# Performance work log

Measured on AMD Instinct MI355X. Metric: run time of the kernel, lower is better.

The kernel has to match this reference:

```python
import jax, jax.numpy as jnp
import numpy as np

B, T, HU, C = 256, 128, 512, 64

def setup_inputs() -> dict:
    key = jax.random.key(0)
    k = jax.random.split(key, 8)
    H = jax.random.normal(k[0], (B, T, HU), dtype=jnp.float32)
    y = jax.random.randint(k[1], (B, T), 0, C)
    y_len = jax.random.randint(k[2], (B,), 1, T + 1).astype(jnp.int32)
    y_mask = (jnp.arange(T)[None, :] < y_len[:, None]).astype(jnp.float32)
    xav = float(np.sqrt(6.0 / (3 * HU + C)))
    W = jax.random.uniform(k[3], (C, 3 * HU), minval=-xav, maxval=xav, dtype=jnp.float32)
    b = jnp.zeros((C,), dtype=jnp.float32)
    start_transitions = jax.random.uniform(k[4], (C,), minval=-1.0, maxval=1.0, dtype=jnp.float32)
    end_transitions = jax.random.uniform(k[5], (C,), minval=-1.0, maxval=1.0, dtype=jnp.float32)
    transitions = jax.random.uniform(k[6], (C, C), minval=-1.0, maxval=1.0, dtype=jnp.float32)
    return {"H": H, "W": W, "b": b, "start_transitions": start_transitions,
            "end_transitions": end_transitions, "transitions": transitions,
            "y": y, "y_mask": y_mask, "y_len": y_len}

def _crf_ll(H, W, b, start_transitions, end_transitions, transitions, y, y_mask, y_len):
    Bn, Tn, hu = H.shape
    zeros = jnp.zeros((Bn, 1, hu), H.dtype)
    prev = jnp.concatenate([zeros, H[:, :-1, :]], axis=1)
    nxt = jnp.concatenate([H[:, 1:, :], zeros], axis=1)
    context = jnp.concatenate([prev, H, nxt], axis=-1)            # [B,T,3h]
    scores = jnp.einsum('bth,ch->btc', context, W) + b            # [B,T,C]

    # numerator (gold path score)
    em_sel = jnp.take_along_axis(scores, y[..., None], axis=2)[..., 0]  # [B,T]
    num = start_transitions[y[:, 0]]
    num = num + jnp.sum(em_sel[:, :-1] * y_mask[:, :-1], axis=1)
    num = num + jnp.sum(transitions[y[:, :-1], y[:, 1:]] * y_mask[:, 1:], axis=1)
    last_tags = jnp.take_along_axis(y, (y_len - 1)[:, None].astype(y.dtype), axis=1)[:, 0]
    num = num + end_transitions[last_tags]
    num = num + jnp.take_along_axis(scores[:, -1, :], last_tags[:, None], axis=1)[:, 0] * y_mask[:, -1]

    # partition (log Z) via masked logsumexp scan
    em_t = jnp.transpose(scores, (1, 0, 2))   # [T,B,C]
    m_t = y_mask.T                            # [T,B]
    lp0 = start_transitions[None, :] + em_t[0]
    def step(lp, inp):
        em, m = inp
        new = jax.nn.logsumexp(lp[:, :, None] + transitions[None, :, :] + em[:, None, :], axis=1)
        lp = new * m[:, None] + lp * (1.0 - m[:, None])
        return lp, None
    lp, _ = jax.lax.scan(step, lp0, (em_t[1:], m_t[1:]))
    logZ = jax.nn.logsumexp(lp + end_transitions[None, :], axis=1)
    return num - logZ                          # [B]

def reference(H, W, b, start_transitions, end_transitions, transitions, y, y_mask, y_len):
    return _crf_ll(H, W, b, start_transitions, end_transitions, transitions, y, y_mask, y_len)
```

## Files before the change

kernel.cpp:

```cpp
#include <hip/hip_runtime.h>

typedef __attribute__((ext_vector_type(8))) short short8;
typedef __attribute__((ext_vector_type(4))) float f32x4;
typedef __fp16 h2_t __attribute__((ext_vector_type(2)));

__device__ __forceinline__ unsigned pk_rtz(float a, float b) {
  h2_t h = __builtin_amdgcn_cvt_pkrtz(a, b);
  return __builtin_bit_cast(unsigned, h);
}
__device__ __forceinline__ unsigned pk_rne(float a, float b) {
  unsigned short ha = __builtin_bit_cast(unsigned short, (_Float16)a);
  unsigned short hb = __builtin_bit_cast(unsigned short, (_Float16)b);
  return (unsigned)ha | ((unsigned)hb << 16);
}
__device__ __forceinline__ unsigned short f2bf(float x) {
  unsigned int u = __float_as_uint(x);
  u += 0x7FFFu + ((u >> 16) & 1u);
  return (unsigned short)(u >> 16);
}
__device__ __forceinline__ unsigned scale_bf_pair(unsigned w, float s) {
  float f0 = __uint_as_float(w << 16) * s;
  float f1 = __uint_as_float(w & 0xFFFF0000u) * s;
  unsigned r;
  asm("v_cvt_pk_bf16_f32 %0, %1, %2" : "=v"(r) : "v"(f0), "v"(f1));
  return r;
}

__global__ __launch_bounds__(512) void crf_fused_kernel(
    const float* __restrict__ H, const float* __restrict__ W,
    const float* __restrict__ bias,
    const float* __restrict__ startT, const float* __restrict__ endT,
    const float* __restrict__ trans,
    const int* __restrict__ y, const int* __restrict__ y_len,
    float* __restrict__ out)
{
  __shared__ __align__(16) float smem[25088];
  __shared__ __align__(16) unsigned char EAbuf[8192];
  __shared__ __align__(16) float sc[128][68];
  __shared__ float scm[128];
  __shared__ float emy[128];
  __shared__ __align__(16) float ubuf[64];
  unsigned char* aTh = (unsigned char*)smem;
  unsigned char* aTl = aTh + 16384;
  unsigned char* bTh = aTh + 32768;
  float* P = smem;
  unsigned char* Mbase = (unsigned char*)smem;

  const int b    = blockIdx.x;
  const int tid  = threadIdx.x;
  const int lane = tid & 63;
  const int wid  = tid >> 6;
  const int wm   = wid >> 2;
  const int wn   = wid & 3;

  f32x4 acc[4][3] = {};
  const float* Hb = H + (size_t)b * (128 * 512);
  const int len = y_len[b];
  const int* yb = y + b * 128;

  float4 areg[4], breg[6];
  int aRow[4], aK4[4], bN[6], bK4[6];
  #pragma unroll
  for (int it = 0; it < 4; ++it) { int i = it * 512 + tid; aRow[it] = i >> 4; aK4[it] = i & 15; }
  #pragma unroll
  for (int it = 0; it < 6; ++it) { int i = it * 512 + tid; bN[it] = i >> 4; bK4[it] = i & 15; }
  #pragma unroll
  for (int it = 0; it < 4; ++it)
    areg[it] = ((const float4*)(Hb + aRow[it] * 512))[aK4[it]];
  #pragma unroll
  for (int it = 0; it < 6; ++it)
    breg[it] = ((const float4*)(W + (bN[it] & 63) * 1536 + (bN[it] >> 6) * 512))[bK4[it]];

  #pragma unroll
  for (int it = 0; it < 2; ++it) {
    int idx = it * 512 + tid;
    int c = idx >> 4, c4 = idx & 15;
    float4 v = ((const float4*)trans)[idx];
    #pragma unroll
    for (int e = 0; e < 4; ++e) {
      int cp = c4 * 4 + e;
      float val = __expf(((const float*)&v)[e] - 1.0f);
      *(unsigned short*)(EAbuf + cp * 128 + ((2 * c) ^ ((cp & 7) << 4))) = f2bf(val);
    }
  }

  for (int kk = 0; kk < 512; kk += 64) {
    if (kk) __syncthreads();
    #pragma unroll
    for (int it = 0; it < 4; ++it) {
      float4 v = areg[it];
      h2_t h01 = __builtin_amdgcn_cvt_pkrtz(v.x, v.y);
      h2_t h23 = __builtin_amdgcn_cvt_pkrtz(v.z, v.w);
      float r0 = v.x - (float)h01[0];
      float r1 = v.y - (float)h01[1];
      float r2 = v.z - (float)h23[0];
      float r3 = v.w - (float)h23[1];
      uint2 hi; hi.x = __builtin_bit_cast(unsigned, h01); hi.y = __builtin_bit_cast(unsigned, h23);
      uint2 lo; lo.x = pk_rtz(r0, r1); lo.y = pk_rtz(r2, r3);
      int off = aRow[it] * 128 + ((aK4[it] * 8) ^ ((aRow[it] & 7) << 4));
      *(uint2*)(aTh + off) = hi; *(uint2*)(aTl + off) = lo;
    }
    #pragma unroll
    for (int it = 0; it < 6; ++it) {
      float4 v = breg[it];
      uint2 bh; bh.x = pk_rne(v.x, v.y); bh.y = pk_rne(v.z, v.w);
      int off = bN[it] * 128 + ((bK4[it] * 8) ^ ((bN[it] & 7) << 4));
      *(uint2*)(bTh + off) = bh;
    }
    __syncthreads();
    if (kk < 448) {
      #pragma unroll
      for (int it = 0; it < 4; ++it)
        areg[it] = ((const float4*)(Hb + aRow[it] * 512 + kk + 64))[aK4[it]];
      #pragma unroll
      for (int it = 0; it < 6; ++it)
        breg[it] = ((const float4*)(W + (bN[it] & 63) * 1536 + (bN[it] >> 6) * 512 + kk + 64))[bK4[it]];
    }
    #pragma unroll
    for (int ks = 0; ks < 2; ++ks) {
      const int kbyte = ks * 64 + ((lane >> 4) << 4);
      short8 ah[4], al[4], bh[3];
      #pragma unroll
      for (int m = 0; m < 4; ++m) {
        int row = wm * 64 + m * 16 + (lane & 15);
        int off = row * 128 + (kbyte ^ ((row & 7) << 4));
        ah[m] = *(const short8*)(aTh + off);
        al[m] = *(const short8*)(aTl + off);
      }
      #pragma unroll
      for (int n = 0; n < 3; ++n) {
        int col = wn * 48 + n * 16 + (lane & 15);
        int off = col * 128 + (kbyte ^ ((col & 7) << 4));
        bh[n] = *(const short8*)(bTh + off);
      }
      #pragma unroll
      for (int m = 0; m < 4; ++m)
        #pragma unroll
        for (int n = 0; n < 3; ++n) {
          asm("v_mfma_f32_16x16x32_f16 %0, %1, %2, %0"
              : "+v"(acc[m][n]) : "v"(ah[m]), "v"(bh[n]));
          asm("v_mfma_f32_16x16x32_f16 %0, %1, %2, %0"
              : "+v"(acc[m][n]) : "v"(al[m]), "v"(bh[n]));
        }
    }
  }
  __syncthreads();

  #pragma unroll
  for (int m = 0; m < 4; ++m)
    #pragma unroll
    for (int n = 0; n < 3; ++n) {
      int row0 = wm * 64 + m * 16 + ((lane >> 4) << 2);
      int col  = wn * 48 + n * 16 + (lane & 15);
      #pragma unroll
      for (int j = 0; j < 4; ++j)
        P[(row0 + j) * 196 + col] = acc[m][n][j];
    }
  __syncthreads();

  #pragma unroll
  for (int it = 0; it < 4; ++it) {
    int i4 = it * 512 + tid;
    int t = i4 >> 4, c4 = i4 & 15;
    float4 s = *(const float4*)(P + t * 196 + 64 + c4 * 4);
    float4 bb = ((const float4*)bias)[c4];
    s.x += bb.x; s.y += bb.y; s.z += bb.z; s.w += bb.w;
    if (t > 0) {
      float4 g = *(const float4*)(P + (t - 1) * 196 + c4 * 4);
      s.x += g.x; s.y += g.y; s.z += g.z; s.w += g.w;
    }
    if (t < 127) {
      float4 g = *(const float4*)(P + (t + 1) * 196 + 128 + c4 * 4);
      s.x += g.x; s.y += g.y; s.z += g.z; s.w += g.w;
    }
    *(float4*)(&sc[t][c4 * 4]) = s;
    float m4 = fmaxf(fmaxf(s.x, s.y), fmaxf(s.z, s.w));
    #pragma unroll
    for (int o = 1; o < 16; o <<= 1) m4 = fmaxf(m4, __shfl_xor(m4, o, 64));
    if ((lane & 15) == 0) scm[t] = m4;
    int yt = yb[t];
    if ((yt >> 2) == c4) {
      int r = yt & 3;
      emy[t] = (r == 0) ? s.x : (r == 1) ? s.y : (r == 2) ? s.z : s.w;
    }
  }
  __syncthreads();

  {
    int row = tid >> 2, c0 = (tid & 3) << 4;
    float mt = scm[row];
    float4* p4 = (float4*)&sc[row][c0];
    #pragma unroll
    for (int j = 0; j < 4; ++j) {
      float4 x = p4[j];
      x.x = __expf(x.x - mt); x.y = __expf(x.y - mt);
      x.z = __expf(x.z - mt); x.w = __expf(x.w - mt);
      p4[j] = x;
    }
  }
  float num = 0.f;
  if (wid == 0) {
    float p = 0.f;
    #pragma unroll
    for (int rep = 0; rep < 2; ++rep) {
      int t = lane + rep * 64;
      if (t < 127) {
        int yt = yb[t], yt1 = yb[t + 1];
        if (t < len)     p += emy[t];
        if (t + 1 < len) p += trans[yt * 64 + yt1];
      }
    }
    #pragma unroll
    for (int s = 32; s > 0; s >>= 1) p += __shfl_xor(p, s, 64);
    num = p + startT[yb[0]] + endT[yb[len - 1]];
    if (len == 128) num += emy[127];
  }
  __syncthreads();

  {
    unsigned char* Mb = Mbase + wid * 8192;
    int t0 = (wid == 0) ? 1 : 16 * wid;
    int t1 = 16 * wid + 15; if (t1 > len - 1) t1 = len - 1;
    if (t0 <= t1) {
      const int sw = (lane & 7) << 4;
      float s0 = sc[t0][lane];
      #pragma unroll
      for (int j = 0; j < 8; ++j) {
        uint4 w = *(const uint4*)(EAbuf + lane * 128 + ((j * 16) ^ sw));
        uint4 o;
        o.x = scale_bf_pair(w.x, s0); o.y = scale_bf_pair(w.y, s0);
        o.z = scale_bf_pair(w.z, s0); o.w = scale_bf_pair(w.w, s0);
        *(uint4*)(Mb + lane * 128 + ((j * 16) ^ sw)) = o;
      }
      short8 ea[4][2];
      #pragma unroll
      for (int rt = 0; rt < 4; ++rt)
        #pragma unroll
        for (int kh = 0; kh < 2; ++kh) {
          int row = rt * 16 + (lane & 15);
          int kb = kh * 64 + ((lane >> 4) << 4);
          ea[rt][kh] = *(const short8*)(EAbuf + row * 128 + (kb ^ ((row & 7) << 4)));
        }
      f32x4 z4 = {0.f, 0.f, 0.f, 0.f};
      for (int t = t0 + 1; t <= t1; ++t) {
        short8 mf[4][2];
        #pragma unroll
        for (int ct = 0; ct < 4; ++ct)
          #pragma unroll
          for (int kh = 0; kh < 2; ++kh) {
            int row = ct * 16 + (lane & 15);
            int kb = kh * 64 + ((lane >> 4) << 4);
            mf[ct][kh] = *(const short8*)(Mb + row * 128 + (kb ^ ((row & 7) << 4)));
          }
        f32x4 sv[4];
        #pragma unroll
        for (int rt = 0; rt < 4; ++rt)
          sv[rt] = *(const f32x4*)(&sc[t][rt * 16 + ((lane >> 4) << 2)]);
        f32x4 c[4][4];
        #pragma unroll
        for (int rt = 0; rt < 4; ++rt)
          #pragma unroll
          for (int ct = 0; ct < 4; ++ct) {
            asm("v_mfma_f32_16x16x32_bf16 %0, %1, %2, %3"
                : "=&v"(c[rt][ct]) : "v"(ea[rt][0]), "v"(mf[ct][0]), "v"(z4));
            asm("v_mfma_f32_16x16x32_bf16 %0, %1, %2, %0"
                : "+v"(c[rt][ct]) : "v"(ea[rt][1]), "v"(mf[ct][1]));
          }
        #pragma unroll
        for (int rt = 0; rt < 4; ++rt)
          #pragma unroll
          for (int ct = 0; ct < 4; ++ct) {
            f32x4 cc = c[rt][ct] * sv[rt];
            unsigned p0, p1;
            asm("v_cvt_pk_bf16_f32 %0, %1, %2" : "=v"(p0) : "v"(cc[0]), "v"(cc[1]));
            asm("v_cvt_pk_bf16_f32 %0, %1, %2" : "=v"(p1) : "v"(cc[2]), "v"(cc[3]));
            uint2 w2; w2.x = p0; w2.y = p1;
            int row = ct * 16 + (lane & 15);
            int byt = 2 * (rt * 16 + ((lane >> 4) << 2));
            *(uint2*)(Mb + row * 128 + (byt ^ ((row & 7) << 4))) = w2;
          }
      }
    }
  }
  __syncthreads();
  if (wid != 0) return;

  float eE = __expf(endT[lane]);
  float ls;
  {
    int t1 = 1 + lane, t2 = 65 + lane;
    float a = (t1 <= len - 1) ? (scm[t1] + 1.0f) : 0.f;
    if (t2 <= len - 1) a += scm[t2] + 1.0f;
    #pragma unroll
    for (int s = 32; s > 0; s >>= 1) a += __shfl_xor(a, s, 64);
    ls = a + scm[0];
  }
  float u = __expf(startT[lane]) * sc[0][lane];

  for (int k = 0; k < 8; ++k) {
    if (16 * k >= len) break;
    int lo = (k == 0) ? 1 : 16 * k;
    int hi = 16 * k + 15; if (hi > len - 1) hi = len - 1;
    if (lo > hi) continue;
    float r = u;
    #pragma unroll
    for (int s = 32; s > 0; s >>= 1) r = fmaxf(r, __shfl_xor(r, s, 64));
    unsigned br = __float_as_uint(r) & 0x7F800000u;
    u *= __uint_as_float(0x7F000000u - br);
    ls += (float)((int)(br >> 23) - 127) * 0.69314718055994531f;
    const unsigned char* Mb = Mbase + k * 8192;
    ubuf[lane] = u;
    float v = 0.f;
    #pragma unroll 4
    for (int c = 0; c < 64; c += 4) {
      float4 uu = *(const float4*)&ubuf[c];
      float m0 = __uint_as_float(((unsigned)*(const unsigned short*)(Mb + (c + 0) * 128 + ((2 * lane) ^ (((c + 0) & 7) << 4)))) << 16);
      float m1 = __uint_as_float(((unsigned)*(const unsigned short*)(Mb + (c + 1) * 128 + ((2 * lane) ^ (((c + 1) & 7) << 4)))) << 16);
      float m2 = __uint_as_float(((unsigned)*(const unsigned short*)(Mb + (c + 2) * 128 + ((2 * lane) ^ (((c + 2) & 7) << 4)))) << 16);
      float m3 = __uint_as_float(((unsigned)*(const unsigned short*)(Mb + (c + 3) * 128 + ((2 * lane) ^ (((c + 3) & 7) << 4)))) << 16);
      v = fmaf(uu.x, m0, v);
      v = fmaf(uu.y, m1, v);
      v = fmaf(uu.z, m2, v);
      v = fmaf(uu.w, m3, v);
    }
    u = v;
  }

  float x = u * eE;
  #pragma unroll
  for (int s = 32; s > 0; s >>= 1) x += __shfl_xor(x, s, 64);
  if (lane == 0) out[b] = num - (__logf(x) + ls);
}

extern "C" void kernel_launch(void* const* d_in, const int* in_sizes, int n_in,
                              void* d_out, int out_size, void* d_ws, size_t ws_size,
                              hipStream_t stream) {
  const float* H      = (const float*)d_in[0];
  const float* W      = (const float*)d_in[1];
  const float* bias   = (const float*)d_in[2];
  const float* startT = (const float*)d_in[3];
  const float* endT   = (const float*)d_in[4];
  const float* trans  = (const float*)d_in[5];
  const int*   y      = (const int*)d_in[6];
  const int*   y_len  = (const int*)d_in[8];
  float* out = (float*)d_out;

  crf_fused_kernel<<<dim3(256), dim3(512), 0, stream>>>(
      H, W, bias, startT, endT, trans, y, y_len, out);
}
```

Measured before the change: 46.31 us.

## Split CRF scan into 16 chunks of 8 steps, two per wave, bf16 score buffer

```diff
diff --git a/kernel.cpp b/kernel.cpp
--- a/kernel.cpp
+++ b/kernel.cpp
@@ -18,12 +18,18 @@
   u += 0x7FFFu + ((u >> 16) & 1u);
   return (unsigned short)(u >> 16);
 }
+__device__ __forceinline__ float bf2f(unsigned short h) {
+  return __uint_as_float(((unsigned)h) << 16);
+}
+__device__ __forceinline__ unsigned pk_bf(float a, float b) {
+  unsigned r;
+  asm("v_cvt_pk_bf16_f32 %0, %1, %2" : "=v"(r) : "v"(a), "v"(b));
+  return r;
+}
 __device__ __forceinline__ unsigned scale_bf_pair(unsigned w, float s) {
   float f0 = __uint_as_float(w << 16) * s;
   float f1 = __uint_as_float(w & 0xFFFF0000u) * s;
-  unsigned r;
-  asm("v_cvt_pk_bf16_f32 %0, %1, %2" : "=v"(r) : "v"(f0), "v"(f1));
-  return r;
+  return pk_bf(f0, f1);
 }
 
 __global__ __launch_bounds__(512) void crf_fused_kernel(
@@ -34,12 +40,13 @@
     const int* __restrict__ y, const int* __restrict__ y_len,
     float* __restrict__ out)
 {
-  __shared__ __align__(16) float smem[25088];
+  __shared__ __align__(16) float smem[32768];
   __shared__ __align__(16) unsigned char EAbuf[8192];
-  __shared__ __align__(16) float sc[128][68];
+  __shared__ __align__(16) unsigned short scbf[128][64];
   __shared__ float scm[128];
   __shared__ float emy[128];
   __shared__ __align__(16) float ubuf[64];
+  __shared__ float numsh;
   unsigned char* aTh = (unsigned char*)smem;
   unsigned char* aTl = aTh + 16384;
   unsigned char* bTh = aTh + 32768;
@@ -173,7 +180,6 @@
       float4 g = *(const float4*)(P + (t + 1) * 196 + 128 + c4 * 4);
       s.x += g.x; s.y += g.y; s.z += g.z; s.w += g.w;
     }
-    *(float4*)(&sc[t][c4 * 4]) = s;
     float m4 = fmaxf(fmaxf(s.x, s.y), fmaxf(s.z, s.w));
     #pragma unroll
     for (int o = 1; o < 16; o <<= 1) m4 = fmaxf(m4, __shfl_xor(m4, o, 64));
@@ -183,23 +189,14 @@
       int r = yt & 3;
       emy[t] = (r == 0) ? s.x : (r == 1) ? s.y : (r == 2) ? s.z : s.w;
     }
+    float e0 = __expf(s.x - m4), e1 = __expf(s.y - m4);
+    float e2 = __expf(s.z - m4), e3 = __expf(s.w - m4);
+    uint2 w2; w2.x = pk_bf(e0, e1); w2.y = pk_bf(e2, e3);
+    *(uint2*)&scbf[t][c4 * 4] = w2;
   }
   __syncthreads();
 
-  {
-    int row = tid >> 2, c0 = (tid & 3) << 4;
-    float mt = scm[row];
-    float4* p4 = (float4*)&sc[row][c0];
-    #pragma unroll
-    for (int j = 0; j < 4; ++j) {
-      float4 x = p4[j];
-      x.x = __expf(x.x - mt); x.y = __expf(x.y - mt);
-      x.z = __expf(x.z - mt); x.w = __expf(x.w - mt);
-      p4[j] = x;
-    }
-  }
-  float num = 0.f;
-  if (wid == 0) {
+  if (wid == 7) {
     float p = 0.f;
     #pragma unroll
     for (int rep = 0; rep < 2; ++rep) {
@@ -212,73 +209,128 @@
     }
     #pragma unroll
     for (int s = 32; s > 0; s >>= 1) p += __shfl_xor(p, s, 64);
-    num = p + startT[yb[0]] + endT[yb[len - 1]];
-    if (len == 128) num += emy[127];
-  }
-  __syncthreads();
+    float nm = p + startT[yb[0]] + endT[yb[len - 1]];
+    if (len == 128) nm += emy[127];
+    if (lane == 0) numsh = nm;
+  }
 
   {
-    unsigned char* Mb = Mbase + wid * 8192;
-    int t0 = (wid == 0) ? 1 : 16 * wid;
-    int t1 = 16 * wid + 15; if (t1 > len - 1) t1 = len - 1;
-    if (t0 <= t1) {
-      const int sw = (lane & 7) << 4;
-      float s0 = sc[t0][lane];
+    short8 ea[4][2];
+    #pragma unroll
+    for (int rt = 0; rt < 4; ++rt)
+      #pragma unroll
+      for (int kh = 0; kh < 2; ++kh) {
+        int row = rt * 16 + (lane & 15);
+        int kb = kh * 64 + ((lane >> 4) << 4);
+        ea[rt][kh] = *(const short8*)(EAbuf + row * 128 + (kb ^ ((row & 7) << 4)));
+      }
+    f32x4 z4 = {0.f, 0.f, 0.f, 0.f};
+
+    const int cA = wid, cB = wid + 8;
+    unsigned char* MbA = Mbase + cA * 8192;
+    unsigned char* MbB = Mbase + cB * 8192;
+    const int t0A = (cA == 0) ? 1 : 8 * cA;
+    const int t1A = (8 * cA + 7 < len - 1) ? 8 * cA + 7 : len - 1;
+    const int t0B = 8 * cB;
+    const int t1B = (8 * cB + 7 < len - 1) ? 8 * cB + 7 : len - 1;
+    const int sw2 = (lane & 7) << 4;
+
+    if (t0A <= t1A) {
+      float s0 = bf2f(scbf[t0A][lane]);
       #pragma unroll
       for (int j = 0; j < 8; ++j) {
-        uint4 w = *(const uint4*)(EAbuf + lane * 128 + ((j * 16) ^ sw));
+        uint4 w = *(const uint4*)(EAbuf + lane * 128 + ((j * 16) ^ sw2));
         uint4 o;
         o.x = scale_bf_pair(w.x, s0); o.y = scale_bf_pair(w.y, s0);
         o.z = scale_bf_pair(w.z, s0); o.w = scale_bf_pair(w.w, s0);
-        *(uint4*)(Mb + lane * 128 + ((j * 16) ^ sw)) = o;
-      }
-      short8 ea[4][2];
-      #pragma unroll
-      for (int rt = 0; rt < 4; ++rt)
+        *(uint4*)(MbA + lane * 128 + ((j * 16) ^ sw2)) = o;
+      }
+    }
+    if (t0B <= t1B) {
+      float s0 = bf2f(scbf[t0B][lane]);
+      #pragma unroll
+      for (int j = 0; j < 8; ++j) {
+        uint4 w = *(const uint4*)(EAbuf + lane * 128 + ((j * 16) ^ sw2));
+        uint4 o;
+        o.x = scale_bf_pair(w.x, s0); o.y = scale_bf_pair(w.y, s0);
+        o.z = scale_bf_pair(w.z, s0); o.w = scale_bf_pair(w.w, s0);
+        *(uint4*)(MbB + lane * 128 + ((j * 16) ^ sw2)) = o;
+      }
+    }
+
+    #pragma unroll 1
+    for (int i = 1; i <= 7; ++i) {
+      int tA = t0A + i, tB = t0B + i;
+      bool dA = (tA <= t1A), dB = (tB <= t1B);
+      short8 mfA[4][2], mfB[4][2];
+      #pragma unroll
+      for (int ct = 0; ct < 4; ++ct)
         #pragma unroll
         for (int kh = 0; kh < 2; ++kh) {
-          int row = rt * 16 + (lane & 15);
+          int row = ct * 16 + (lane & 15);
           int kb = kh * 64 + ((lane >> 4) << 4);
-          ea[rt][kh] = *(const short8*)(EAbuf + row * 128 + (kb ^ ((row & 7) << 4)));
+          int off = row * 128 + (kb ^ ((row & 7) << 4));
+          mfA[ct][kh] = *(const short8*)(MbA + off);
+          mfB[ct][kh] = *(const short8*)(MbB + off);
         }
-      f32x4 z4 = {0.f, 0.f, 0.f, 0.f};
-      for (int t = t0 + 1; t <= t1; ++t) {
-        short8 mf[4][2];
-        #pragma unroll
-        for (int ct = 0; ct < 4; ++ct)
-          #pragma unroll
-          for (int kh = 0; kh < 2; ++kh) {
-            int row = ct * 16 + (lane & 15);
-            int kb = kh * 64 + ((lane >> 4) << 4);
-            mf[ct][kh] = *(const short8*)(Mb + row * 128 + (kb ^ ((row & 7) << 4)));
-          }
-        f32x4 sv[4];
-        #pragma unroll
-        for (int rt = 0; rt < 4; ++rt)
-          sv[rt] = *(const f32x4*)(&sc[t][rt * 16 + ((lane >> 4) << 2)]);
+      f32x4 svA[4], svB[4];
+      #pragma unroll
+      for (int rt = 0; rt < 4; ++rt) {
+        int cidx = rt * 16 + ((lane >> 4) << 2);
+        ushort4 ra = *(const ushort4*)&scbf[tA][cidx];
+        ushort4 rb = *(const ushort4*)&scbf[tB][cidx];
+        svA[rt][0] = bf2f(ra.x); svA[rt][1] = bf2f(ra.y);
+        svA[rt][2] = bf2f(ra.z); svA[rt][3] = bf2f(ra.w);
+        svB[rt][0] = bf2f(rb.x); svB[rt][1] = bf2f(rb.y);
+        svB[rt][2] = bf2f(rb.z); svB[rt][3] = bf2f(rb.w);
+      }
+      {
         f32x4 c[4][4];
         #pragma unroll
         for (int rt = 0; rt < 4; ++rt)
           #pragma unroll
           for (int ct = 0; ct < 4; ++ct) {
             asm("v_mfma_f32_16x16x32_bf16 %0, %1, %2, %3"
-                : "=&v"(c[rt][ct]) : "v"(ea[rt][0]), "v"(mf[ct][0]), "v"(z4));
+                : "=&v"(c[rt][ct]) : "v"(ea[rt][0]), "v"(mfA[ct][0]), "v"(z4));
             asm("v_mfma_f32_16x16x32_bf16 %0, %1, %2, %0"
-                : "+v"(c[rt][ct]) : "v"(ea[rt][1]), "v"(mf[ct][1]));
+                : "+v"(c[rt][ct]) : "v"(ea[rt][1]), "v"(mfA[ct][1]));
           }
+        if (dA) {
+          #pragma unroll
+          for (int rt = 0; rt < 4; ++rt)
+            #pragma unroll
+            for (int ct = 0; ct < 4; ++ct) {
+              f32x4 cc = c[rt][ct] * svA[rt];
+              uint2 w2; w2.x = pk_bf(cc[0], cc[1]); w2.y = pk_bf(cc[2], cc[3]);
+              int row = ct * 16 + (lane & 15);
+              int byt = 2 * (rt * 16 + ((lane >> 4) << 2));
+              *(uint2*)(MbA + row * 128 + (byt ^ ((row & 7) << 4))) = w2;
+            }
+        }
+      }
+      {
+        f32x4 c[4][4];
         #pragma unroll
         for (int rt = 0; rt < 4; ++rt)
           #pragma unroll
           for (int ct = 0; ct < 4; ++ct) {
-            f32x4 cc = c[rt][ct] * sv[rt];
-            unsigned p0, p1;
-            asm("v_cvt_pk_bf16_f32 %0, %1, %2" : "=v"(p0) : "v"(cc[0]), "v"(cc[1]));
-            asm("v_cvt_pk_bf16_f32 %0, %1, %2" : "=v"(p1) : "v"(cc[2]), "v"(cc[3]));
-            uint2 w2; w2.x = p0; w2.y = p1;
-            int row = ct * 16 + (lane & 15);
-            int byt = 2 * (rt * 16 + ((lane >> 4) << 2));
-            *(uint2*)(Mb + row * 128 + (byt ^ ((row & 7) << 4))) = w2;
+            asm("v_mfma_f32_16x16x32_bf16 %0, %1, %2, %3"
+                : "=&v"(c[rt][ct]) : "v"(ea[rt][0]), "v"(mfB[ct][0]), "v"(z4));
+            asm("v_mfma_f32_16x16x32_bf16 %0, %1, %2, %0"
+                : "+v"(c[rt][ct]) : "v"(ea[rt][1]), "v"(mfB[ct][1]));
           }
+        if (dB) {
+          #pragma unroll
+          for (int rt = 0; rt < 4; ++rt)
+            #pragma unroll
+            for (int ct = 0; ct < 4; ++ct) {
+              f32x4 cc = c[rt][ct] * svB[rt];
+              uint2 w2; w2.x = pk_bf(cc[0], cc[1]); w2.y = pk_bf(cc[2], cc[3]);
+              int row = ct * 16 + (lane & 15);
+              int byt = 2 * (rt * 16 + ((lane >> 4) << 2));
+              *(uint2*)(MbB + row * 128 + (byt ^ ((row & 7) << 4))) = w2;
+            }
+        }
       }
     }
   }
@@ -295,12 +347,12 @@
     for (int s = 32; s > 0; s >>= 1) a += __shfl_xor(a, s, 64);
     ls = a + scm[0];
   }
-  float u = __expf(startT[lane]) * sc[0][lane];
-
-  for (int k = 0; k < 8; ++k) {
-    if (16 * k >= len) break;
-    int lo = (k == 0) ? 1 : 16 * k;
-    int hi = 16 * k + 15; if (hi > len - 1) hi = len - 1;
+  float u = __expf(startT[lane]) * bf2f(scbf[0][lane]);
+
+  for (int k = 0; k < 16; ++k) {
+    if (k && 8 * k >= len) break;
+    int lo = (k == 0) ? 1 : 8 * k;
+    int hi = 8 * k + 7; if (hi > len - 1) hi = len - 1;
     if (lo > hi) continue;
     float r = u;
     #pragma unroll
@@ -310,26 +362,26 @@
     ls += (float)((int)(br >> 23) - 127) * 0.69314718055994531f;
     const unsigned char* Mb = Mbase + k * 8192;
     ubuf[lane] = u;
-    float v = 0.f;
+    float v0 = 0.f, v1 = 0.f, v2 = 0.f, v3 = 0.f;
     #pragma unroll 4
     for (int c = 0; c < 64; c += 4) {
       float4 uu = *(const float4*)&ubuf[c];
-      float m0 = __uint_as_float(((unsigned)*(const unsigned short*)(Mb + (c + 0) * 128 + ((2 * lane) ^ (((c + 0) & 7) << 4)))) << 16);
-      float m1 = __uint_as_float(((unsigned)*(const unsigned short*)(Mb + (c + 1) * 128 + ((2 * lane) ^ (((c + 1) & 7) << 4)))) << 16);
-      float m2 = __uint_as_float(((unsigned)*(const unsigned short*)(Mb + (c + 2) * 128 + ((2 * lane) ^ (((c + 2) & 7) << 4)))) << 16);
-      float m3 = __uint_as_float(((unsigned)*(const unsigned short*)(Mb + (c + 3) * 128 + ((2 * lane) ^ (((c + 3) & 7) << 4)))) << 16);
-      v = fmaf(uu.x, m0, v);
-      v = fmaf(uu.y, m1, v);
-      v = fmaf(uu.z, m2, v);
-      v = fmaf(uu.w, m3, v);
-    }
-    u = v;
+      float m0 = bf2f(*(const unsigned short*)(Mb + (c + 0) * 128 + ((2 * lane) ^ (((c + 0) & 7) << 4))));
+      float m1 = bf2f(*(const unsigned short*)(Mb + (c + 1) * 128 + ((2 * lane) ^ (((c + 1) & 7) << 4))));
+      float m2 = bf2f(*(const unsigned short*)(Mb + (c + 2) * 128 + ((2 * lane) ^ (((c + 2) & 7) << 4))));
+      float m3 = bf2f(*(const unsigned short*)(Mb + (c + 3) * 128 + ((2 * lane) ^ (((c + 3) & 7) << 4))));
+      v0 = fmaf(uu.x, m0, v0);
+      v1 = fmaf(uu.y, m1, v1);
+      v2 = fmaf(uu.z, m2, v2);
+      v3 = fmaf(uu.w, m3, v3);
+    }
+    u = (v0 + v1) + (v2 + v3);
   }
 
   float x = u * eE;
   #pragma unroll
   for (int s = 32; s > 0; s >>= 1) x += __shfl_xor(x, s, 64);
-  if (lane == 0) out[b] = num - (__logf(x) + ls);
+  if (lane == 0) out[b] = numsh - (__logf(x) + ls);
 }
 
 extern "C" void kernel_launch(void* const* d_in, const int* in_sizes, int n_in,
```

Result: slower. 52.74 us (+13.9%).

## Drop split-fp16 low residual in emission GEMM and split final chain accumulators

Applied to the files above, without the earlier changes.

```diff
diff --git a/kernel.cpp b/kernel.cpp
--- a/kernel.cpp
+++ b/kernel.cpp
@@ -2,12 +2,7 @@
 
 typedef __attribute__((ext_vector_type(8))) short short8;
 typedef __attribute__((ext_vector_type(4))) float f32x4;
-typedef __fp16 h2_t __attribute__((ext_vector_type(2)));
-
-__device__ __forceinline__ unsigned pk_rtz(float a, float b) {
-  h2_t h = __builtin_amdgcn_cvt_pkrtz(a, b);
-  return __builtin_bit_cast(unsigned, h);
-}
+
 __device__ __forceinline__ unsigned pk_rne(float a, float b) {
   unsigned short ha = __builtin_bit_cast(unsigned short, (_Float16)a);
   unsigned short hb = __builtin_bit_cast(unsigned short, (_Float16)b);
@@ -18,12 +13,18 @@
   u += 0x7FFFu + ((u >> 16) & 1u);
   return (unsigned short)(u >> 16);
 }
+__device__ __forceinline__ float bf2f(unsigned short h) {
+  return __uint_as_float(((unsigned)h) << 16);
+}
+__device__ __forceinline__ unsigned pk_bf(float a, float b) {
+  unsigned r;
+  asm("v_cvt_pk_bf16_f32 %0, %1, %2" : "=v"(r) : "v"(a), "v"(b));
+  return r;
+}
 __device__ __forceinline__ unsigned scale_bf_pair(unsigned w, float s) {
   float f0 = __uint_as_float(w << 16) * s;
   float f1 = __uint_as_float(w & 0xFFFF0000u) * s;
-  unsigned r;
-  asm("v_cvt_pk_bf16_f32 %0, %1, %2" : "=v"(r) : "v"(f0), "v"(f1));
-  return r;
+  return pk_bf(f0, f1);
 }
 
 __global__ __launch_bounds__(512) void crf_fused_kernel(
@@ -41,8 +42,7 @@
   __shared__ float emy[128];
   __shared__ __align__(16) float ubuf[64];
   unsigned char* aTh = (unsigned char*)smem;
-  unsigned char* aTl = aTh + 16384;
-  unsigned char* bTh = aTh + 32768;
+  unsigned char* bTh = aTh + 16384;
   float* P = smem;
   unsigned char* Mbase = (unsigned char*)smem;
 
@@ -89,16 +89,9 @@
     #pragma unroll
     for (int it = 0; it < 4; ++it) {
       float4 v = areg[it];
-      h2_t h01 = __builtin_amdgcn_cvt_pkrtz(v.x, v.y);
-      h2_t h23 = __builtin_amdgcn_cvt_pkrtz(v.z, v.w);
-      float r0 = v.x - (float)h01[0];
-      float r1 = v.y - (float)h01[1];
-      float r2 = v.z - (float)h23[0];
-      float r3 = v.w - (float)h23[1];
-      uint2 hi; hi.x = __builtin_bit_cast(unsigned, h01); hi.y = __builtin_bit_cast(unsigned, h23);
-      uint2 lo; lo.x = pk_rtz(r0, r1); lo.y = pk_rtz(r2, r3);
+      uint2 hi; hi.x = pk_rne(v.x, v.y); hi.y = pk_rne(v.z, v.w);
       int off = aRow[it] * 128 + ((aK4[it] * 8) ^ ((aRow[it] & 7) << 4));
-      *(uint2*)(aTh + off) = hi; *(uint2*)(aTl + off) = lo;
+      *(uint2*)(aTh + off) = hi;
     }
     #pragma unroll
     for (int it = 0; it < 6; ++it) {
@@ -119,29 +112,23 @@
     #pragma unroll
     for (int ks = 0; ks < 2; ++ks) {
       const int kbyte = ks * 64 + ((lane >> 4) << 4);
-      short8 ah[4], al[4], bh[3];
+      short8 ah[4], bh[3];
       #pragma unroll
       for (int m = 0; m < 4; ++m) {
         int row = wm * 64 + m * 16 + (lane & 15);
-        int off = row * 128 + (kbyte ^ ((row & 7) << 4));
-        ah[m] = *(const short8*)(aTh + off);
-        al[m] = *(const short8*)(aTl + off);
+        ah[m] = *(const short8*)(aTh + row * 128 + (kbyte ^ ((row & 7) << 4)));
       }
       #pragma unroll
       for (int n = 0; n < 3; ++n) {
         int col = wn * 48 + n * 16 + (lane & 15);
-        int off = col * 128 + (kbyte ^ ((col & 7) << 4));
-        bh[n] = *(const short8*)(bTh + off);
+        bh[n] = *(const short8*)(bTh + col * 128 + (kbyte ^ ((col & 7) << 4)));
       }
       #pragma unroll
       for (int m = 0; m < 4; ++m)
         #pragma unroll
-        for (int n = 0; n < 3; ++n) {
+        for (int n = 0; n < 3; ++n)
           asm("v_mfma_f32_16x16x32_f16 %0, %1, %2, %0"
               : "+v"(acc[m][n]) : "v"(ah[m]), "v"(bh[n]));
-          asm("v_mfma_f32_16x16x32_f16 %0, %1, %2, %0"
-              : "+v"(acc[m][n]) : "v"(al[m]), "v"(bh[n]));
-        }
     }
   }
   __syncthreads();
@@ -271,10 +258,7 @@
           #pragma unroll
           for (int ct = 0; ct < 4; ++ct) {
             f32x4 cc = c[rt][ct] * sv[rt];
-            unsigned p0, p1;
-            asm("v_cvt_pk_bf16_f32 %0, %1, %2" : "=v"(p0) : "v"(cc[0]), "v"(cc[1]));
-            asm("v_cvt_pk_bf16_f32 %0, %1, %2" : "=v"(p1) : "v"(cc[2]), "v"(cc[3]));
-            uint2 w2; w2.x = p0; w2.y = p1;
+            uint2 w2; w2.x = pk_bf(cc[0], cc[1]); w2.y = pk_bf(cc[2], cc[3]);
             int row = ct * 16 + (lane & 15);
             int byt = 2 * (rt * 16 + ((lane >> 4) << 2));
             *(uint2*)(Mb + row * 128 + (byt ^ ((row & 7) << 4))) = w2;
@@ -298,7 +282,7 @@
   float u = __expf(startT[lane]) * sc[0][lane];
 
   for (int k = 0; k < 8; ++k) {
-    if (16 * k >= len) break;
+    if (k && 16 * k >= len) break;
     int lo = (k == 0) ? 1 : 16 * k;
     int hi = 16 * k + 15; if (hi > len - 1) hi = len - 1;
     if (lo > hi) continue;
@@ -310,20 +294,20 @@
     ls += (float)((int)(br >> 23) - 127) * 0.69314718055994531f;
     const unsigned char* Mb = Mbase + k * 8192;
     ubuf[lane] = u;
-    float v = 0.f;
+    float v0 = 0.f, v1 = 0.f, v2 = 0.f, v3 = 0.f;
     #pragma unroll 4
     for (int c = 0; c < 64; c += 4) {
       float4 uu = *(const float4*)&ubuf[c];
-      float m0 = __uint_as_float(((unsigned)*(const unsigned short*)(Mb + (c + 0) * 128 + ((2 * lane) ^ (((c + 0) & 7) << 4)))) << 16);
-      float m1 = __uint_as_float(((unsigned)*(const unsigned short*)(Mb + (c + 1) * 128 + ((2 * lane) ^ (((c + 1) & 7) << 4)))) << 16);
-      float m2 = __uint_as_float(((unsigned)*(const unsigned short*)(Mb + (c + 2) * 128 + ((2 * lane) ^ (((c + 2) & 7) << 4)))) << 16);
-      float m3 = __uint_as_float(((unsigned)*(const unsigned short*)(Mb + (c + 3) * 128 + ((2 * lane) ^ (((c + 3) & 7) << 4)))) << 16);
-      v = fmaf(uu.x, m0, v);
-      v = fmaf(uu.y, m1, v);
-      v = fmaf(uu.z, m2, v);
-      v = fmaf(uu.w, m3, v);
-    }
-    u = v;
+      float m0 = bf2f(*(const unsigned short*)(Mb + (c + 0) * 128 + ((2 * lane) ^ (((c + 0) & 7) << 4))));
+      float m1 = bf2f(*(const unsigned short*)(Mb + (c + 1) * 128 + ((2 * lane) ^ (((c + 1) & 7) << 4))));
+      float m2 = bf2f(*(const unsigned short*)(Mb + (c + 2) * 128 + ((2 * lane) ^ (((c + 2) & 7) << 4))));
+      float m3 = bf2f(*(const unsigned short*)(Mb + (c + 3) * 128 + ((2 * lane) ^ (((c + 3) & 7) << 4))));
+      v0 = fmaf(uu.x, m0, v0);
+      v1 = fmaf(uu.y, m1, v1);
+      v2 = fmaf(uu.z, m2, v2);
+      v3 = fmaf(uu.w, m3, v3);
+    }
+    u = (v0 + v1) + (v2 + v3);
   }
 
   float x = u * eE;
```

New measurement: 43.75 us. -5.5%, faster.
